# Optimization experiments

Measured on AMD Instinct MI355X. Metric: run time of the kernel, lower is better.

The kernel has to match this reference:

```python
import jax, jax.numpy as jnp
import numpy as np

D = 1024
H = 16
HD = D // H


def setup_inputs() -> dict:
    key = jax.random.key(0)
    ks = jax.random.split(key, 5)
    s = 1.0 / np.sqrt(D)
    return {
        "inputs": jax.random.normal(ks[0], (2, 2048, D), dtype=jnp.float32),
        "Wq": jax.random.normal(ks[1], (D, D), dtype=jnp.float32) * s,
        "bq": jnp.zeros((D,), jnp.float32),
        "Wk": jax.random.normal(ks[2], (D, D), dtype=jnp.float32) * s,
        "bk": jnp.zeros((D,), jnp.float32),
        "Wv": jax.random.normal(ks[3], (D, D), dtype=jnp.float32) * s,
        "bv": jnp.zeros((D,), jnp.float32),
        "Wo": jax.random.normal(ks[4], (D, D), dtype=jnp.float32) * s,
        "bo": jnp.zeros((D,), jnp.float32),
    }


def reference(inputs, Wq, bq, Wk, bk, Wv, bv, Wo, bo):
    B, S, _ = inputs.shape
    def split_heads(x):  # [B,S,D] -> [B,H,S,hd]
        return x.reshape(B, S, H, HD).transpose(0, 2, 1, 3)
    q = split_heads(inputs @ Wq + bq)
    k = split_heads(inputs @ Wk + bk)
    v = split_heads(inputs @ Wv + bv)
    scale = 1.0 / jnp.sqrt(jnp.asarray(HD, inputs.dtype))
    scores = jnp.einsum("bhsd,bhtd->bhst", q, k) * scale  # [B,H,S,S]
    weights = jax.nn.softmax(scores, axis=-1)
    attn = jnp.einsum("bhst,bhtd->bhsd", weights, v)
    concat = attn.transpose(0, 2, 1, 3).reshape(B, S, D)
    return concat @ Wo + bo
```

## Files before the change

### kernel.cpp

```cpp
#include <hip/hip_runtime.h>


typedef __bf16 bf16x8 __attribute__((ext_vector_type(8)));
typedef float  f32x4  __attribute__((ext_vector_type(4)));

#if __has_builtin(__builtin_amdgcn_exp2f)
#define EXPFN(x) __builtin_amdgcn_exp2f(x)
#define QSCALE (0.125f * 1.44269504088896f)
#else
#define EXPFN(x) __expf(x)
#define QSCALE 0.125f
#endif

#define LDKP 74

__device__ __forceinline__ unsigned short f2bf(float f) {
    unsigned int u = __float_as_uint(f);
    u += 0x7FFFu + ((u >> 16) & 1u);
    return (unsigned short)(u >> 16);
}

__device__ __forceinline__ void gload16(const void* g, void* l) {
    __builtin_amdgcn_global_load_lds(
        (const __attribute__((address_space(1))) void*)g,
        (__attribute__((address_space(3))) void*)l, 16, 0, 0);
}

#define WAIT0_BARRIER() asm volatile("s_waitcnt vmcnt(0)\n\ts_barrier" ::: "memory")

__global__ __launch_bounds__(256) void cast_x_kernel(
    const float4* __restrict__ X, ushort4* __restrict__ Xb, int n4) {
    int i = blockIdx.x * 256 + threadIdx.x;
    if (i < n4) {
        float4 v = X[i];
        ushort4 o;
        o.x = f2bf(v.x); o.y = f2bf(v.y); o.z = f2bf(v.z); o.w = f2bf(v.w);
        Xb[i] = o;
    }
}

__global__ __launch_bounds__(256) void transpose_w_kernel(
    const float* __restrict__ Wq, const float* __restrict__ Wk,
    const float* __restrict__ Wv, const float* __restrict__ Wo,
    unsigned short* __restrict__ Wt_all) {
    __shared__ float tile[32][33];
    const int z = blockIdx.z;
    const float* W = (z == 0) ? Wq : (z == 1) ? Wk : (z == 2) ? Wv : Wo;
    unsigned short* Wt = Wt_all + (size_t)z * 1024 * 1024;
    int c0 = blockIdx.x * 32, r0 = blockIdx.y * 32;
    int x = threadIdx.x, y = threadIdx.y;
    for (int j = 0; j < 32; j += 8)
        tile[y + j][x] = W[(r0 + y + j) * 1024 + c0 + x];
    __syncthreads();
    for (int j = 0; j < 32; j += 8)
        Wt[(c0 + y + j) * 1024 + r0 + x] = f2bf(tile[x][y + j]);
}

__global__ __launch_bounds__(256) void gemm_qkv_kernel(
    const unsigned short* __restrict__ Xb, const unsigned short* __restrict__ Wt_all,
    const float* __restrict__ bq, const float* __restrict__ bk,
    const float* __restrict__ bv,
    unsigned short* __restrict__ Qb, unsigned short* __restrict__ Kb,
    unsigned short* __restrict__ Vt) {
    const int z = blockIdx.z;
    const int x0 = blockIdx.x * 128;
    const int y0 = blockIdx.y * 128;

    const unsigned short* Ap;
    const unsigned short* Bp;
    if (z < 2) {
        Ap = Xb + (size_t)x0 * 1024;
        Bp = Wt_all + (size_t)z * 1024 * 1024 + (size_t)y0 * 1024;
    } else {
        Ap = Wt_all + (size_t)2 * 1024 * 1024 + (size_t)y0 * 1024;
        Bp = Xb + (size_t)x0 * 1024;
    }

    __shared__ __align__(16) unsigned short As[2][128 * 64];
    __shared__ __align__(16) unsigned short Bs[2][128 * 64];

    const int tid = threadIdx.x;
    const int lane = tid & 63, wave = tid >> 6;
    const int quad = lane >> 4, l15 = lane & 15;
    const int wrow = (wave >> 1) * 64, wcol = (wave & 1) * 64;

    f32x4 acc[4][4] = {};

    const int srow = lane >> 3;
    const int ch8  = (lane & 7) * 8;
    const int swz  = (((lane & 7) ^ srow)) * 8;
    const int sw   = (l15 & 7);

    #pragma unroll
    for (int c = 0; c < 4; c++) {
        int r = c * 32 + wave * 8 + srow;
        gload16(Ap + (size_t)r * 1024 + 0 + swz, &As[0][r * 64 + ch8]);
        gload16(Bp + (size_t)r * 1024 + 0 + swz, &Bs[0][r * 64 + ch8]);
    }

    for (int k = 0; k < 16; k++) {
        const int cur = k & 1, nxt = cur ^ 1;
        WAIT0_BARRIER();
        if (k < 15) {
            int k0 = (k + 1) * 64;
            #pragma unroll
            for (int c = 0; c < 4; c++) {
                int r = c * 32 + wave * 8 + srow;
                gload16(Ap + (size_t)r * 1024 + k0 + swz, &As[nxt][r * 64 + ch8]);
                gload16(Bp + (size_t)r * 1024 + k0 + swz, &Bs[nxt][r * 64 + ch8]);
            }
        }
        #pragma unroll
        for (int kk = 0; kk < 2; kk++) {
            bf16x8 af[4], bfr[4];
            #pragma unroll
            for (int i = 0; i < 4; i++)
                af[i] = *(const bf16x8*)&As[cur][(wrow + i * 16 + l15) * 64 +
                                                (((kk * 4 + quad) ^ sw)) * 8];
            #pragma unroll
            for (int j = 0; j < 4; j++)
                bfr[j] = *(const bf16x8*)&Bs[cur][(wcol + j * 16 + l15) * 64 +
                                                 (((kk * 4 + quad) ^ sw)) * 8];
            #pragma unroll
            for (int i = 0; i < 4; i++)
                #pragma unroll
                for (int j = 0; j < 4; j++)
                    acc[i][j] = __builtin_amdgcn_mfma_f32_16x16x32_bf16(
                        af[i], bfr[j], acc[i][j], 0, 0, 0);
        }
    }

    if (z < 2) {
        const float* bias = (z == 0) ? bq : bk;
        #pragma unroll
        for (int j = 0; j < 4; j++) {
            int col = y0 + wcol + j * 16 + l15;
            float bcol = bias[col];
            int h = col >> 6, d = col & 63;
            #pragma unroll
            for (int i = 0; i < 4; i++)
                #pragma unroll
                for (int r = 0; r < 4; r++) {
                    int row = x0 + wrow + i * 16 + quad * 4 + r;
                    int b = row >> 11, s = row & 2047;
                    float v = acc[i][j][r] + bcol;
                    if (z == 0)
                        Qb[(size_t)((b * 16 + h) * 2048 + s) * 64 + d] = f2bf(v * QSCALE);
                    else
                        Kb[(size_t)((b * 16 + h) * 2048 + s) * 64 + d] = f2bf(v);
                }
        }
    } else {
        #pragma unroll
        for (int i = 0; i < 4; i++)
            #pragma unroll
            for (int r = 0; r < 4; r++) {
                int rowd = y0 + wrow + i * 16 + quad * 4 + r;
                float brow = bv[rowd];
                #pragma unroll
                for (int j = 0; j < 4; j++) {
                    int colm = x0 + wcol + j * 16 + l15;
                    int b = colm >> 11, s = colm & 2047;
                    Vt[(size_t)(b * 1024 + rowd) * 2048 + s] = f2bf(acc[i][j][r] + brow);
                }
            }
    }
}

__global__ __launch_bounds__(256) void attn_kernel(
    const unsigned short* __restrict__ Qb, const unsigned short* __restrict__ Kb,
    const unsigned short* __restrict__ Vt, unsigned short* __restrict__ Cc,
    float* __restrict__ Op, float* __restrict__ Lp, int tlen, int do_split) {
    const int bh = blockIdx.y;
    const int b = bh >> 4, h = bh & 15;
    const int q0 = blockIdx.x * 128;
    const int split = blockIdx.z;
    const int tbeg = split * tlen;

    const int tid = threadIdx.x;
    const int lane = tid & 63, wave = tid >> 6;
    const int quad = lane >> 4, l15 = lane & 15;

    __shared__ __align__(16) unsigned short Ks[64 * 64];
    __shared__ __align__(16) unsigned short Vs[64 * 64];
    __shared__ __align__(16) unsigned short Ps[4][32 * LDKP];

    const unsigned short* Qbh = Qb + (size_t)bh * 2048 * 64;
    const unsigned short* Kbh = Kb + (size_t)bh * 2048 * 64;
    const unsigned short* Vbh = Vt + (size_t)bh * 64 * 2048;

    bf16x8 qa[2][2];
    #pragma unroll
    for (int mi = 0; mi < 2; mi++)
        #pragma unroll
        for (int kk = 0; kk < 2; kk++)
            qa[mi][kk] = *(const bf16x8*)&Qbh[
                (size_t)(q0 + wave * 32 + mi * 16 + l15) * 64 + kk * 32 + quad * 8];

    union { unsigned short us[8]; bf16x8 v; } ones_u;
    #pragma unroll
    for (int i = 0; i < 8; i++) ones_u.us[i] = 0x3F80;
    const bf16x8 onesv = ones_u.v;

    f32x4 o[2][4] = {};
    f32x4 ol[2] = {};

    const int srow = lane >> 3;
    const int r0s = wave * 16 + srow;
    const int ch8 = (lane & 7) * 8;
    const int swz = (((lane & 7) ^ srow)) * 8;
    const int sw  = (l15 & 7);

    for (int ti = 0; ti < tlen; ti += 64) {
        const int t0 = tbeg + ti;
        __syncthreads();
        gload16(&Kbh[(size_t)(t0 + r0s) * 64 + swz],       &Ks[r0s * 64 + ch8]);
        gload16(&Kbh[(size_t)(t0 + r0s + 8) * 64 + swz],   &Ks[(r0s + 8) * 64 + ch8]);
        gload16(&Vbh[(size_t)r0s * 2048 + t0 + swz],       &Vs[r0s * 64 + ch8]);
        gload16(&Vbh[(size_t)(r0s + 8) * 2048 + t0 + swz], &Vs[(r0s + 8) * 64 + ch8]);
        asm volatile("s_waitcnt vmcnt(0)" ::: "memory");
        __syncthreads();

        f32x4 sf[2][4] = {};
        #pragma unroll
        for (int j = 0; j < 4; j++)
            #pragma unroll
            for (int kk = 0; kk < 2; kk++) {
                bf16x8 kf = *(const bf16x8*)&Ks[(j * 16 + l15) * 64 +
                                                (((kk * 4 + quad) ^ sw)) * 8];
                sf[0][j] = __builtin_amdgcn_mfma_f32_16x16x32_bf16(qa[0][kk], kf, sf[0][j], 0, 0, 0);
                sf[1][j] = __builtin_amdgcn_mfma_f32_16x16x32_bf16(qa[1][kk], kf, sf[1][j], 0, 0, 0);
            }

        #pragma unroll
        for (int mi = 0; mi < 2; mi++)
            #pragma unroll
            for (int j = 0; j < 4; j++)
                #pragma unroll
                for (int r = 0; r < 4; r++) {
                    float p = EXPFN(sf[mi][j][r]);
                    Ps[wave][(mi * 16 + quad * 4 + r) * LDKP + j * 16 + l15] =
                        (unsigned short)(__float_as_uint(p) >> 16);
                }

        asm volatile("s_waitcnt lgkmcnt(0)" ::: "memory");

        #pragma unroll
        for (int kk = 0; kk < 2; kk++) {
            bf16x8 pf0 = *(const bf16x8*)&Ps[wave][(l15) * LDKP + kk * 32 + quad * 8];
            bf16x8 pf1 = *(const bf16x8*)&Ps[wave][(16 + l15) * LDKP + kk * 32 + quad * 8];
            ol[0] = __builtin_amdgcn_mfma_f32_16x16x32_bf16(pf0, onesv, ol[0], 0, 0, 0);
            ol[1] = __builtin_amdgcn_mfma_f32_16x16x32_bf16(pf1, onesv, ol[1], 0, 0, 0);
            #pragma unroll
            for (int j = 0; j < 4; j++) {
                bf16x8 vf = *(const bf16x8*)&Vs[(j * 16 + l15) * 64 +
                                                (((kk * 4 + quad) ^ sw)) * 8];
                o[0][j] = __builtin_amdgcn_mfma_f32_16x16x32_bf16(pf0, vf, o[0][j], 0, 0, 0);
                o[1][j] = __builtin_amdgcn_mfma_f32_16x16x32_bf16(pf1, vf, o[1][j], 0, 0, 0);
            }
        }
    }

    if (do_split) {
        float* Opd = Op + (size_t)(split * 32 + bh) * 2048 * 64;
        float* Lpd = Lp + (size_t)(split * 32 + bh) * 2048;
        #pragma unroll
        for (int mi = 0; mi < 2; mi++)
            #pragma unroll
            for (int r = 0; r < 4; r++) {
                int s = q0 + wave * 32 + mi * 16 + quad * 4 + r;
                if (l15 == 0) Lpd[s] = ol[mi][r];
                #pragma unroll
                for (int j = 0; j < 4; j++)
                    Opd[(size_t)s * 64 + j * 16 + l15] = o[mi][j][r];
            }
    } else {
        #pragma unroll
        for (int mi = 0; mi < 2; mi++)
            #pragma unroll
            for (int r = 0; r < 4; r++) {
                float inv = 1.f / ol[mi][r];
                int s = q0 + wave * 32 + mi * 16 + quad * 4 + r;
                size_t row = (size_t)(b * 2048 + s);
                #pragma unroll
                for (int j = 0; j < 4; j++)
                    Cc[row * 1024 + h * 64 + j * 16 + l15] = f2bf(o[mi][j][r] * inv);
            }
    }
}

__global__ __launch_bounds__(256) void combine_kernel(
    const float4* __restrict__ Op, const float* __restrict__ Lp,
    unsigned short* __restrict__ Cc) {
    int idx = blockIdx.x * 256 + threadIdx.x;
    int d4 = idx & 15;
    int s = (idx >> 4) & 2047;
    int bh = idx >> 15;
    const size_t half4 = (size_t)32 * 2048 * 16;
    float4 a = Op[(size_t)idx], c = Op[half4 + (size_t)idx];
    float l = Lp[bh * 2048 + s] + Lp[32 * 2048 + bh * 2048 + s];
    float inv = 1.f / l;
    ushort4 o;
    o.x = f2bf((a.x + c.x) * inv); o.y = f2bf((a.y + c.y) * inv);
    o.z = f2bf((a.z + c.z) * inv); o.w = f2bf((a.w + c.w) * inv);
    int b = bh >> 4, h = bh & 15;
    *(ushort4*)&Cc[((size_t)(b * 2048 + s)) * 1024 + h * 64 + d4 * 4] = o;
}

__global__ __launch_bounds__(256) void gemm_out_kernel(
    const unsigned short* __restrict__ Cc, const unsigned short* __restrict__ Wot,
    const float* __restrict__ bo, float* __restrict__ out) {
    const int m0 = blockIdx.x * 128;
    const int n0 = blockIdx.y * 64;

    __shared__ __align__(16) unsigned short As[2][128 * 64];
    __shared__ __align__(16) unsigned short Bs[2][64 * 64];

    const int tid = threadIdx.x;
    const int lane = tid & 63, wave = tid >> 6;
    const int quad = lane >> 4, l15 = lane & 15;
    const int wrow = (wave >> 1) * 64, wcol = (wave & 1) * 32;

    f32x4 acc[4][2] = {};
    const int srow = lane >> 3;
    const int ch8 = (lane & 7) * 8;
    const int swz = (((lane & 7) ^ srow)) * 8;
    const int sw  = (l15 & 7);

    #pragma unroll
    for (int c = 0; c < 4; c++) {
        int r = c * 32 + wave * 8 + srow;
        gload16(Cc + (size_t)(m0 + r) * 1024 + swz, &As[0][r * 64 + ch8]);
        if (c < 2)
            gload16(Wot + (size_t)(n0 + r) * 1024 + swz, &Bs[0][r * 64 + ch8]);
    }

    for (int k = 0; k < 16; k++) {
        const int cur = k & 1, nxt = cur ^ 1;
        WAIT0_BARRIER();
        if (k < 15) {
            int k0 = (k + 1) * 64;
            #pragma unroll
            for (int c = 0; c < 4; c++) {
                int r = c * 32 + wave * 8 + srow;
                gload16(Cc + (size_t)(m0 + r) * 1024 + k0 + swz, &As[nxt][r * 64 + ch8]);
                if (c < 2)
                    gload16(Wot + (size_t)(n0 + r) * 1024 + k0 + swz, &Bs[nxt][r * 64 + ch8]);
            }
        }
        #pragma unroll
        for (int kk = 0; kk < 2; kk++) {
            bf16x8 af[4], bfr[2];
            #pragma unroll
            for (int i = 0; i < 4; i++)
                af[i] = *(const bf16x8*)&As[cur][(wrow + i * 16 + l15) * 64 +
                                                (((kk * 4 + quad) ^ sw)) * 8];
            #pragma unroll
            for (int j = 0; j < 2; j++)
                bfr[j] = *(const bf16x8*)&Bs[cur][(wcol + j * 16 + l15) * 64 +
                                                 (((kk * 4 + quad) ^ sw)) * 8];
            #pragma unroll
            for (int i = 0; i < 4; i++)
                #pragma unroll
                for (int j = 0; j < 2; j++)
                    acc[i][j] = __builtin_amdgcn_mfma_f32_16x16x32_bf16(
                        af[i], bfr[j], acc[i][j], 0, 0, 0);
        }
    }

    #pragma unroll
    for (int j = 0; j < 2; j++) {
        int col = n0 + wcol + j * 16 + l15;
        float bcol = bo[col];
        #pragma unroll
        for (int i = 0; i < 4; i++)
            #pragma unroll
            for (int r = 0; r < 4; r++) {
                int row = m0 + wrow + i * 16 + quad * 4 + r;
                out[(size_t)row * 1024 + col] = acc[i][j][r] + bcol;
            }
    }
}

extern "C" void kernel_launch(void* const* d_in, const int* in_sizes, int n_in,
                              void* d_out, int out_size, void* d_ws, size_t ws_size,
                              hipStream_t stream) {
    const float* X  = (const float*)d_in[0];
    const float* Wq = (const float*)d_in[1];
    const float* bq = (const float*)d_in[2];
    const float* Wk = (const float*)d_in[3];
    const float* bk = (const float*)d_in[4];
    const float* Wv = (const float*)d_in[5];
    const float* bv = (const float*)d_in[6];
    const float* Wo = (const float*)d_in[7];
    const float* bo = (const float*)d_in[8];
    float* out = (float*)d_out;

    char* ws = (char*)d_ws;
    unsigned short* Xb = (unsigned short*)(ws);
    unsigned short* Wt = (unsigned short*)(ws + (8u  << 20));
    unsigned short* Qb = (unsigned short*)(ws + (16u << 20));
    unsigned short* Kb = (unsigned short*)(ws + (24u << 20));
    unsigned short* Vt = (unsigned short*)(ws + (32u << 20));
    unsigned short* Cc = (unsigned short*)(ws + (40u << 20));
    float* Op = (float*)(ws + (48u << 20));
    float* Lp = (float*)(ws + (48u << 20) + 33554432u);
    const bool use_split = ws_size >= ((size_t)(48u << 20) + 33554432u + 524288u);

    cast_x_kernel<<<4096, 256, 0, stream>>>((const float4*)X, (ushort4*)Xb, 1048576);
    transpose_w_kernel<<<dim3(32, 32, 4), dim3(32, 8), 0, stream>>>(Wq, Wk, Wv, Wo, Wt);
    gemm_qkv_kernel<<<dim3(32, 8, 3), 256, 0, stream>>>(Xb, Wt, bq, bk, bv, Qb, Kb, Vt);
    if (use_split) {
        attn_kernel<<<dim3(16, 32, 2), 256, 0, stream>>>(Qb, Kb, Vt, Cc, Op, Lp, 1024, 1);
        combine_kernel<<<4096, 256, 0, stream>>>((const float4*)Op, Lp, Cc);
    } else {
        attn_kernel<<<dim3(16, 32, 1), 256, 0, stream>>>(Qb, Kb, Vt, Cc, Op, Lp, 2048, 0);
    }
    gemm_out_kernel<<<dim3(32, 16), 256, 0, stream>>>(Cc, Wt + 3u * 1024 * 1024, bo, out);
}
```

Before: 205.5 us.

## Halve GEMM K-tile to 32 and widen output GEMM tile to 128x128

Both the QKV and output-projection GEMMs now stage 32-wide K slices instead of 64, with a new XOR swizzle for the narrower LDS rows. This halves LDS usage per block so more blocks can be resident, at the cost of twice as many barrier iterations. The output GEMM tile grows from 128x64 to 128x128 with a 4x4 MFMA accumulator per wave, which improves operand reuse but halves the grid to 256 blocks.

```diff
diff --git a/kernel.cpp b/kernel.cpp
--- a/kernel.cpp
+++ b/kernel.cpp
@@ -76,8 +76,8 @@
         Bp = Xb + (size_t)x0 * 1024;
     }
 
-    __shared__ __align__(16) unsigned short As[2][128 * 64];
-    __shared__ __align__(16) unsigned short Bs[2][128 * 64];
+    __shared__ __align__(16) unsigned short As[2][128 * 32];
+    __shared__ __align__(16) unsigned short Bs[2][128 * 32];
 
     const int tid = threadIdx.x;
     const int lane = tid & 63, wave = tid >> 6;
@@ -86,48 +86,45 @@
 
     f32x4 acc[4][4] = {};
 
-    const int srow = lane >> 3;
-    const int ch8  = (lane & 7) * 8;
-    const int swz  = (((lane & 7) ^ srow)) * 8;
-    const int sw   = (l15 & 7);
+    const int srow = lane >> 2;
+    const int ch4  = (lane & 3) * 8;
+    const int sw4  = (((lane & 3) ^ (srow & 3) ^ ((srow >> 2) & 3))) * 8;
+    const int rsw  = (l15 & 3) ^ ((l15 >> 2) & 3);
 
     #pragma unroll
-    for (int c = 0; c < 4; c++) {
-        int r = c * 32 + wave * 8 + srow;
-        gload16(Ap + (size_t)r * 1024 + 0 + swz, &As[0][r * 64 + ch8]);
-        gload16(Bp + (size_t)r * 1024 + 0 + swz, &Bs[0][r * 64 + ch8]);
-    }
-
-    for (int k = 0; k < 16; k++) {
+    for (int c = 0; c < 2; c++) {
+        int r = c * 64 + wave * 16 + srow;
+        gload16(Ap + (size_t)r * 1024 + 0 + sw4, &As[0][r * 32 + ch4]);
+        gload16(Bp + (size_t)r * 1024 + 0 + sw4, &Bs[0][r * 32 + ch4]);
+    }
+
+    for (int k = 0; k < 32; k++) {
         const int cur = k & 1, nxt = cur ^ 1;
         WAIT0_BARRIER();
-        if (k < 15) {
-            int k0 = (k + 1) * 64;
-            #pragma unroll
-            for (int c = 0; c < 4; c++) {
-                int r = c * 32 + wave * 8 + srow;
-                gload16(Ap + (size_t)r * 1024 + k0 + swz, &As[nxt][r * 64 + ch8]);
-                gload16(Bp + (size_t)r * 1024 + k0 + swz, &Bs[nxt][r * 64 + ch8]);
+        if (k < 31) {
+            int k0 = (k + 1) * 32;
+            #pragma unroll
+            for (int c = 0; c < 2; c++) {
+                int r = c * 64 + wave * 16 + srow;
+                gload16(Ap + (size_t)r * 1024 + k0 + sw4, &As[nxt][r * 32 + ch4]);
+                gload16(Bp + (size_t)r * 1024 + k0 + sw4, &Bs[nxt][r * 32 + ch4]);
             }
         }
-        #pragma unroll
-        for (int kk = 0; kk < 2; kk++) {
-            bf16x8 af[4], bfr[4];
-            #pragma unroll
-            for (int i = 0; i < 4; i++)
-                af[i] = *(const bf16x8*)&As[cur][(wrow + i * 16 + l15) * 64 +
-                                                (((kk * 4 + quad) ^ sw)) * 8];
+        bf16x8 af[4], bfr[4];
+        #pragma unroll
+        for (int i = 0; i < 4; i++)
+            af[i] = *(const bf16x8*)&As[cur][(wrow + i * 16 + l15) * 32 +
+                                             ((quad ^ rsw)) * 8];
+        #pragma unroll
+        for (int j = 0; j < 4; j++)
+            bfr[j] = *(const bf16x8*)&Bs[cur][(wcol + j * 16 + l15) * 32 +
+                                              ((quad ^ rsw)) * 8];
+        #pragma unroll
+        for (int i = 0; i < 4; i++)
             #pragma unroll
             for (int j = 0; j < 4; j++)
-                bfr[j] = *(const bf16x8*)&Bs[cur][(wcol + j * 16 + l15) * 64 +
-                                                 (((kk * 4 + quad) ^ sw)) * 8];
-            #pragma unroll
-            for (int i = 0; i < 4; i++)
-                #pragma unroll
-                for (int j = 0; j < 4; j++)
-                    acc[i][j] = __builtin_amdgcn_mfma_f32_16x16x32_bf16(
-                        af[i], bfr[j], acc[i][j], 0, 0, 0);
-        }
+                acc[i][j] = __builtin_amdgcn_mfma_f32_16x16x32_bf16(
+                    af[i], bfr[j], acc[i][j], 0, 0, 0);
     }
 
     if (z < 2) {
@@ -311,65 +308,60 @@
     const unsigned short* __restrict__ Cc, const unsigned short* __restrict__ Wot,
     const float* __restrict__ bo, float* __restrict__ out) {
     const int m0 = blockIdx.x * 128;
-    const int n0 = blockIdx.y * 64;
-
-    __shared__ __align__(16) unsigned short As[2][128 * 64];
-    __shared__ __align__(16) unsigned short Bs[2][64 * 64];
+    const int n0 = blockIdx.y * 128;
+
+    __shared__ __align__(16) unsigned short As[2][128 * 32];
+    __shared__ __align__(16) unsigned short Bs[2][128 * 32];
 
     const int tid = threadIdx.x;
     const int lane = tid & 63, wave = tid >> 6;
     const int quad = lane >> 4, l15 = lane & 15;
-    const int wrow = (wave >> 1) * 64, wcol = (wave & 1) * 32;
-
-    f32x4 acc[4][2] = {};
-    const int srow = lane >> 3;
-    const int ch8 = (lane & 7) * 8;
-    const int swz = (((lane & 7) ^ srow)) * 8;
-    const int sw  = (l15 & 7);
+    const int wrow = (wave >> 1) * 64, wcol = (wave & 1) * 64;
+
+    f32x4 acc[4][4] = {};
+    const int srow = lane >> 2;
+    const int ch4  = (lane & 3) * 8;
+    const int sw4  = (((lane & 3) ^ (srow & 3) ^ ((srow >> 2) & 3))) * 8;
+    const int rsw  = (l15 & 3) ^ ((l15 >> 2) & 3);
 
     #pragma unroll
-    for (int c = 0; c < 4; c++) {
-        int r = c * 32 + wave * 8 + srow;
-        gload16(Cc + (size_t)(m0 + r) * 1024 + swz, &As[0][r * 64 + ch8]);
-        if (c < 2)
-            gload16(Wot + (size_t)(n0 + r) * 1024 + swz, &Bs[0][r * 64 + ch8]);
-    }
-
-    for (int k = 0; k < 16; k++) {
+    for (int c = 0; c < 2; c++) {
+        int r = c * 64 + wave * 16 + srow;
+        gload16(Cc + (size_t)(m0 + r) * 1024 + sw4,  &As[0][r * 32 + ch4]);
+        gload16(Wot + (size_t)(n0 + r) * 1024 + sw4, &Bs[0][r * 32 + ch4]);
+    }
+
+    for (int k = 0; k < 32; k++) {
         const int cur = k & 1, nxt = cur ^ 1;
         WAIT0_BARRIER();
-        if (k < 15) {
-            int k0 = (k + 1) * 64;
-            #pragma unroll
-            for (int c = 0; c < 4; c++) {
-                int r = c * 32 + wave * 8 + srow;
-                gload16(Cc + (size_t)(m0 + r) * 1024 + k0 + swz, &As[nxt][r * 64 + ch8]);
-                if (c < 2)
-                    gload16(Wot + (size_t)(n0 + r) * 1024 + k0 + swz, &Bs[nxt][r * 64 + ch8]);
+        if (k < 31) {
+            int k0 = (k + 1) * 32;
+            #pragma unroll
+            for (int c = 0; c < 2; c++) {
+                int r = c * 64 + wave * 16 + srow;
+                gload16(Cc + (size_t)(m0 + r) * 1024 + k0 + sw4,  &As[nxt][r * 32 + ch4]);
+                gload16(Wot + (size_t)(n0 + r) * 1024 + k0 + sw4, &Bs[nxt][r * 32 + ch4]);
             }
         }
-        #pragma unroll
-        for (int kk = 0; kk < 2; kk++) {
-            bf16x8 af[4], bfr[2];
-            #pragma unroll
-            for (int i = 0; i < 4; i++)
-                af[i] = *(const bf16x8*)&As[cur][(wrow + i * 16 + l15) * 64 +
-                                                (((kk * 4 + quad) ^ sw)) * 8];
-            #pragma unroll
-            for (int j = 0; j < 2; j++)
-                bfr[j] = *(const bf16x8*)&Bs[cur][(wcol + j * 16 + l15) * 64 +
-                                                 (((kk * 4 + quad) ^ sw)) * 8];
-            #pragma unroll
-            for (int i = 0; i < 4; i++)
-                #pragma unroll
-                for (int j = 0; j < 2; j++)
-                    acc[i][j] = __builtin_amdgcn_mfma_f32_16x16x32_bf16(
-                        af[i], bfr[j], acc[i][j], 0, 0, 0);
-        }
+        bf16x8 af[4], bfr[4];
+        #pragma unroll
+        for (int i = 0; i < 4; i++)
+            af[i] = *(const bf16x8*)&As[cur][(wrow + i * 16 + l15) * 32 +
+                                             ((quad ^ rsw)) * 8];
+        #pragma unroll
+        for (int j = 0; j < 4; j++)
+            bfr[j] = *(const bf16x8*)&Bs[cur][(wcol + j * 16 + l15) * 32 +
+                                              ((quad ^ rsw)) * 8];
+        #pragma unroll
+        for (int i = 0; i < 4; i++)
+            #pragma unroll
+            for (int j = 0; j < 4; j++)
+                acc[i][j] = __builtin_amdgcn_mfma_f32_16x16x32_bf16(
+                    af[i], bfr[j], acc[i][j], 0, 0, 0);
     }
 
     #pragma unroll
-    for (int j = 0; j < 2; j++) {
+    for (int j = 0; j < 4; j++) {
         int col = n0 + wcol + j * 16 + l15;
         float bcol = bo[col];
         #pragma unroll
@@ -416,5 +408,5 @@
     } else {
         attn_kernel<<<dim3(16, 32, 1), 256, 0, stream>>>(Qb, Kb, Vt, Cc, Op, Lp, 2048, 0);
     }
-    gemm_out_kernel<<<dim3(32, 16), 256, 0, stream>>>(Cc, Wt + 3u * 1024 * 1024, bo, out);
-}
+    gemm_out_kernel<<<dim3(32, 8), 256, 0, stream>>>(Cc, Wt + 3u * 1024 * 1024, bo, out);
+}
```

Measured after the change: 225.8 us. 1.1x slower.
